# Kernel optimization log

Measured on AMD Instinct MI355X. Metric: run time of the kernel, lower is better.

## Reference

```python
import jax, jax.numpy as jnp
import numpy as np


def setup_inputs() -> dict:
    key = jax.random.key(0)
    ks = jax.random.split(key, 6)
    B, T, Dz, Dc, K, R = 64, 2048, 512, 256, 12, 2
    z = jax.random.normal(ks[0], (B, T, Dz), jnp.float32)
    c = jax.random.normal(ks[1], (B, T, Dc), jnp.float32)
    # per-step Linear(256 -> 512): weight (out, in) and bias, like nn.Linear
    Wk_w = jax.random.normal(ks[2], (K, Dz, Dc), jnp.float32) / np.sqrt(Dc)
    Wk_b = jax.random.normal(ks[3], (K, Dz), jnp.float32) * 0.01
    # random anchor time per batch element, t in [0, T - K - 1)
    t = jax.random.randint(ks[4], (B,), 0, T - K - 1)
    # negative-sampling indices: per step k and replicate r, T-1 draws with
    # replacement from the T-1 non-positive frames (same vector for all batches)
    rand_idx = jax.random.randint(ks[5], (K, R, T - 1), 0, T - 1)
    return {"z": z, "c": c, "Wk_w": Wk_w, "Wk_b": Wk_b,
            "t": t, "rand_idx": rand_idx, "n_replicates": R}


def reference(z, c, Wk_w, Wk_b, t, rand_idx, n_replicates):
    B, T, Dz = z.shape
    K = Wk_w.shape[0]
    steps = jnp.arange(1, K + 1)  # k = 1..K
    # c_t: context at anchor time -> (B, Dc)
    c_t = jnp.take_along_axis(c, t[:, None, None], axis=1)[:, 0, :]
    # pred_k = Wk[k](c_t): (K, B, Dz)
    pred = jnp.einsum('bd,kod->kbo', c_t, Wk_w) + Wk_b[:, None, :]
    # scores of every frame against pred (avoids the original's O(B^2) matmul
    # whose diagonal is extracted): (K, B, T)
    s = jnp.einsum('btd,kbd->kbt', z, pred)
    # positive index t_i + k per (k, batch)
    e = t[None, :] + steps[:, None]                      # (K, B)
    pos = jnp.take_along_axis(s, e[:, :, None], axis=2)[:, :, 0]  # (K, B)
    # map a draw j in [0, T-1) onto frame indices skipping the positive frame
    skip = (rand_idx[:, None, :, :] >= e[:, :, None, None]).astype(rand_idx.dtype)
    actual = rand_idx[:, None, :, :] + skip              # (K, B, R, T-1)
    neg = jnp.take_along_axis(s[:, :, None, :], actual, axis=3)  # (K, B, R, T-1)
    R = neg.shape[2]
    # candidate 0 is the positive, then T-1 negatives
    fk = jnp.concatenate(
        [jnp.broadcast_to(pos[:, :, None, None], (K, B, R, 1)), neg], axis=3)
    log_sm = jax.nn.log_softmax(fk, axis=3)
    per_kb = jnp.mean(log_sm[:, :, :, 0], axis=2)        # mean over replicates
    loss = (-per_kb).mean(axis=0).sum() / B              # mean over k, mean over batch
    return loss
```

## Files before the change

### kernel.cpp

```cpp
#include <hip/hip_runtime.h>
#include <math.h>

#define B_  64
#define T_  2048
#define DZ_ 512
#define DC_ 256
#define K_  12
#define R_  2

__global__ __launch_bounds__(256) void pred_kernel(
    const float* __restrict__ c, const float* __restrict__ W,
    const float* __restrict__ bias, const int* __restrict__ t,
    float* __restrict__ pred)
{
    __shared__ float cts[8 * DC_];
    const int oz = blockIdx.x;
    const int b0 = blockIdx.y * 8;
    const int k  = blockIdx.z;
    const int tid = threadIdx.x;

    for (int i = tid; i < 8 * DC_; i += 256) {
        int bb = i >> 8;
        int d  = i & 255;
        int tb = t[b0 + bb];
        cts[i] = c[((size_t)(b0 + bb) * T_ + tb) * DC_ + d];
    }
    __syncthreads();

    const int o = oz * 256 + tid;
    const float4* W4   = (const float4*)(W + ((size_t)k * DZ_ + o) * DC_);
    const float4* cts4 = (const float4*)cts;

    float acc[8];
    #pragma unroll
    for (int bb = 0; bb < 8; ++bb) acc[bb] = 0.f;

    for (int d4 = 0; d4 < DC_ / 4; ++d4) {
        float4 w = W4[d4];
        #pragma unroll
        for (int bb = 0; bb < 8; ++bb) {
            float4 cv = cts4[bb * (DC_ / 4) + d4];
            acc[bb] += w.x * cv.x + w.y * cv.y + w.z * cv.z + w.w * cv.w;
        }
    }

    const float bv = bias[(size_t)k * DZ_ + o];
    #pragma unroll
    for (int bb = 0; bb < 8; ++bb)
        pred[((size_t)(b0 + bb) * K_ + k) * DZ_ + o] = acc[bb] + bv;
}

#define ROWS_PB 64
__global__ __launch_bounds__(256) void score_kernel(
    const float* __restrict__ z, const float* __restrict__ pred,
    float* __restrict__ s)
{
    __shared__ float ps[K_ * DZ_];
    const int b   = blockIdx.y;
    const int tid = threadIdx.x;

    const float4* pg  = (const float4*)(pred + (size_t)b * K_ * DZ_);
    float4*       ps4s = (float4*)ps;
    for (int i = tid; i < K_ * DZ_ / 4; i += 256) ps4s[i] = pg[i];
    __syncthreads();

    const int wave = tid >> 6, lane = tid & 63;
    const int row0 = blockIdx.x * ROWS_PB + wave * (ROWS_PB / 4);
    const float4* ps4 = (const float4*)ps;

    for (int r = 0; r < ROWS_PB / 4; ++r) {
        const int row = row0 + r;
        const float4* zr = (const float4*)(z + ((size_t)b * T_ + row) * DZ_);
        float4 z0 = zr[lane];
        float4 z1 = zr[lane + 64];

        float acc[K_];
        #pragma unroll
        for (int k = 0; k < K_; ++k) {
            float4 p0 = ps4[k * (DZ_ / 4) + lane];
            float4 p1 = ps4[k * (DZ_ / 4) + lane + 64];
            acc[k] = z0.x * p0.x + z0.y * p0.y + z0.z * p0.z + z0.w * p0.w
                   + z1.x * p1.x + z1.y * p1.y + z1.z * p1.z + z1.w * p1.w;
        }

        #pragma unroll
        for (int k = 0; k < K_; ++k) {
            float v = acc[k];
            #pragma unroll
            for (int off = 32; off >= 1; off >>= 1)
                v += __shfl_xor(v, off, 64);
            acc[k] = v;
        }

        if (lane == 0) {
            #pragma unroll
            for (int k = 0; k < K_; ++k)
                s[((size_t)k * B_ + b) * T_ + row] = acc[k];
        }
    }
}

__global__ __launch_bounds__(256) void loss_kernel(
    const float* __restrict__ s, const int* __restrict__ t,
    const int* __restrict__ rand_idx, float* __restrict__ out)
{
    __shared__ float srow[T_];
    __shared__ float red_m[4], red_l[4];
    const int k   = blockIdx.x;
    const int b   = blockIdx.y;
    const int tid = threadIdx.x;

    const float4* sg = (const float4*)(s + ((size_t)k * B_ + b) * T_);
    float4* s4 = (float4*)srow;
    for (int i = tid; i < T_ / 4; i += 256) s4[i] = sg[i];
    __syncthreads();

    const int e   = t[b] + k + 1;
    const float pos = srow[e];
    float total = 0.f;

    for (int r = 0; r < R_; ++r) {
        const int* ri = rand_idx + ((size_t)k * R_ + r) * (T_ - 1);
        float m = -INFINITY, l = 0.f;
        for (int j = tid; j < T_ - 1; j += 256) {
            int idx = ri[j];
            idx += (idx >= e);
            float v = srow[idx];
            if (v > m) { l = l * __expf(m - v) + 1.f; m = v; }
            else       { l += __expf(v - m); }
        }
        const int lane = tid & 63, wave = tid >> 6;
        #pragma unroll
        for (int off = 32; off >= 1; off >>= 1) {
            float m2 = __shfl_xor(m, off, 64);
            float l2 = __shfl_xor(l, off, 64);
            float mn = fmaxf(m, m2);
            l = l * __expf(m - mn) + l2 * __expf(m2 - mn);
            m = mn;
        }
        if (lane == 0) { red_m[wave] = m; red_l[wave] = l; }
        __syncthreads();
        if (tid == 0) {
            float M = pos, L = 1.f;
            for (int w = 0; w < 4; ++w) {
                float m2 = red_m[w], l2 = red_l[w];
                float mn = fmaxf(M, m2);
                L = L * __expf(M - mn) + l2 * __expf(m2 - mn);
                M = mn;
            }
            total += (M + __logf(L)) - pos;
        }
        __syncthreads();
    }
    if (tid == 0)
        atomicAdd(out, total * (1.0f / (K_ * B_ * R_)));
}

extern "C" void kernel_launch(void* const* d_in, const int* in_sizes, int n_in,
                              void* d_out, int out_size, void* d_ws, size_t ws_size,
                              hipStream_t stream)
{
    const float* z        = (const float*)d_in[0];
    const float* c        = (const float*)d_in[1];
    const float* Wk_w     = (const float*)d_in[2];
    const float* Wk_b     = (const float*)d_in[3];
    const int*   t        = (const int*)d_in[4];
    const int*   rand_idx = (const int*)d_in[5];
    float* out = (float*)d_out;

    float* pred = (float*)d_ws;
    float* s    = pred + (size_t)B_ * K_ * DZ_;

    hipMemsetAsync(d_out, 0, sizeof(float), stream);

    pred_kernel<<<dim3(2, 8, K_), 256, 0, stream>>>(c, Wk_w, Wk_b, t, pred);
    score_kernel<<<dim3(T_ / ROWS_PB, B_), 256, 0, stream>>>(z, pred, s);
    loss_kernel<<<dim3(K_, B_), 256, 0, stream>>>(s, t, rand_idx, out);
}
```

Before: 479.7 us.

## Restructure score kernel so each lane group handles four rows with partial reductions

The score kernel now assigns 8 lanes per group of 4 rows, with each lane striding over the feature dimension. Each pred float4 read from shared memory is reused across 4 rows, and the cross-lane reduction shrinks from 6 shuffle steps over 64 lanes to 3 steps over 8 lanes. Rows per block double to 128, which halves the grid and raises register pressure from the 48 accumulators. Each lane's z loads are strided, so coalescing is partial: 8 lanes share one 128-byte span per row.

```diff
diff --git a/kernel.cpp b/kernel.cpp
--- a/kernel.cpp
+++ b/kernel.cpp
@@ -50,7 +50,8 @@
         pred[((size_t)(b0 + bb) * K_ + k) * DZ_ + o] = acc[bb] + bv;
 }
 
-#define ROWS_PB 64
+#define WROWS   32
+#define ROWS_PB 128
 __global__ __launch_bounds__(256) void score_kernel(
     const float* __restrict__ z, const float* __restrict__ pred,
     float* __restrict__ s)
@@ -60,43 +61,56 @@
     const int tid = threadIdx.x;
 
     const float4* pg  = (const float4*)(pred + (size_t)b * K_ * DZ_);
-    float4*       ps4s = (float4*)ps;
-    for (int i = tid; i < K_ * DZ_ / 4; i += 256) ps4s[i] = pg[i];
+    float4*       psv = (float4*)ps;
+    for (int i = tid; i < K_ * DZ_ / 4; i += 256) psv[i] = pg[i];
     __syncthreads();
 
     const int wave = tid >> 6, lane = tid & 63;
-    const int row0 = blockIdx.x * ROWS_PB + wave * (ROWS_PB / 4);
-    const float4* ps4 = (const float4*)ps;
+    const int i8   = lane & 7;
+    const int r8   = lane >> 3;
+    const int row0 = blockIdx.x * ROWS_PB + wave * WROWS + r8 * 4;
 
-    for (int r = 0; r < ROWS_PB / 4; ++r) {
-        const int row = row0 + r;
-        const float4* zr = (const float4*)(z + ((size_t)b * T_ + row) * DZ_);
-        float4 z0 = zr[lane];
-        float4 z1 = zr[lane + 64];
+    const float4* zr0 = (const float4*)(z + ((size_t)b * T_ + row0) * DZ_) + i8;
+    const float4* ps4 = (const float4*)ps + i8;
 
-        float acc[K_];
+    float acc[4][K_];
+    #pragma unroll
+    for (int j = 0; j < 4; ++j)
+        #pragma unroll
+        for (int k = 0; k < K_; ++k) acc[j][k] = 0.f;
+
+    #pragma unroll 2
+    for (int it = 0; it < 16; ++it) {
+        float4 zv[4];
+        #pragma unroll
+        for (int j = 0; j < 4; ++j) zv[j] = zr0[j * (DZ_ / 4) + it * 8];
         #pragma unroll
         for (int k = 0; k < K_; ++k) {
-            float4 p0 = ps4[k * (DZ_ / 4) + lane];
-            float4 p1 = ps4[k * (DZ_ / 4) + lane + 64];
-            acc[k] = z0.x * p0.x + z0.y * p0.y + z0.z * p0.z + z0.w * p0.w
-                   + z1.x * p1.x + z1.y * p1.y + z1.z * p1.z + z1.w * p1.w;
+            float4 p = ps4[k * (DZ_ / 4) + it * 8];
+            #pragma unroll
+            for (int j = 0; j < 4; ++j)
+                acc[j][k] += zv[j].x * p.x + zv[j].y * p.y
+                           + zv[j].z * p.z + zv[j].w * p.w;
+        }
+    }
+
+    #pragma unroll
+    for (int j = 0; j < 4; ++j)
+        #pragma unroll
+        for (int k = 0; k < K_; ++k) {
+            float v = acc[j][k];
+            v += __shfl_xor(v, 1, 64);
+            v += __shfl_xor(v, 2, 64);
+            v += __shfl_xor(v, 4, 64);
+            acc[j][k] = v;
         }
 
+    if (i8 == 0) {
         #pragma unroll
-        for (int k = 0; k < K_; ++k) {
-            float v = acc[k];
+        for (int k = 0; k < K_; ++k)
             #pragma unroll
-            for (int off = 32; off >= 1; off >>= 1)
-                v += __shfl_xor(v, off, 64);
-            acc[k] = v;
-        }
-
-        if (lane == 0) {
-            #pragma unroll
-            for (int k = 0; k < K_; ++k)
-                s[((size_t)k * B_ + b) * T_ + row] = acc[k];
-        }
+            for (int j = 0; j < 4; ++j)
+                s[((size_t)k * B_ + b) * T_ + row0 + j] = acc[j][k];
     }
 }
 
```

Measured after the change: 466.0 us. -2.9%, faster.
